# Optimization experiments

Measured on AMD Instinct MI355X. Metric: run time of the kernel, lower is better.

## Reference

```python
import jax, jax.numpy as jnp
import numpy as np

DIM_Q = 512
DIM_K = 512
DIM_V = 512
NUM_HEADS = 8
EPS = 1e-5


def _layer_norm(x, g, b):
    m = jnp.mean(x, axis=-1, keepdims=True)
    v = jnp.mean(jnp.square(x - m), axis=-1, keepdims=True)
    return (x - m) * jax.lax.rsqrt(v + EPS) * g + b


def setup_inputs() -> dict:
    key = jax.random.key(0)
    ks = jax.random.split(key, 12)
    B, Sq, Sk = 32, 512, 512
    s_q = 1.0 / np.sqrt(DIM_Q)
    s_v = 1.0 / np.sqrt(DIM_V)
    return {
        "Q": jax.random.normal(ks[0], (B, Sq, DIM_Q), jnp.float32),
        "K": jax.random.normal(ks[1], (B, Sk, DIM_K), jnp.float32),
        "Wq": jax.random.normal(ks[2], (DIM_Q, DIM_V), jnp.float32) * s_q,
        "bq": jnp.zeros((DIM_V,), jnp.float32),
        "Wk": jax.random.normal(ks[3], (DIM_K, DIM_V), jnp.float32) * s_q,
        "bk": jnp.zeros((DIM_V,), jnp.float32),
        "Wv": jax.random.normal(ks[4], (DIM_K, DIM_V), jnp.float32) * s_q,
        "bv": jnp.zeros((DIM_V,), jnp.float32),
        "Wo": jax.random.normal(ks[5], (DIM_V, DIM_V), jnp.float32) * s_v,
        "bo": jnp.zeros((DIM_V,), jnp.float32),
        "ln0_g": jnp.ones((DIM_V,), jnp.float32),
        "ln0_b": jnp.zeros((DIM_V,), jnp.float32),
        "ln1_g": jnp.ones((DIM_V,), jnp.float32),
        "ln1_b": jnp.zeros((DIM_V,), jnp.float32),
    }


def reference(Q, K, Wq, bq, Wk, bk, Wv, bv, Wo, bo, ln0_g, ln0_b, ln1_g, ln1_b):
    B, Sq, _ = Q.shape
    Sk = K.shape[1]
    H = NUM_HEADS
    dh = DIM_V // H
    q = Q @ Wq + bq  # [B, Sq, V]
    k = K @ Wk + bk  # [B, Sk, V]
    v = K @ Wv + bv  # [B, Sk, V]
    # split(dim_split, 2) + cat(dim 0) == standard head split
    qh = q.reshape(B, Sq, H, dh)
    kh = k.reshape(B, Sk, H, dh)
    vh = v.reshape(B, Sk, H, dh)
    # NOTE: original scales by sqrt(dim_V), not sqrt(head_dim)
    scores = jnp.einsum("bqhd,bkhd->bhqk", qh, kh) / np.sqrt(DIM_V)
    A = jax.nn.softmax(scores, axis=-1)  # [B, H, Sq, Sk]
    oh = qh + jnp.einsum("bhqk,bkhd->bqhd", A, vh)  # residual inside heads
    O = oh.reshape(B, Sq, DIM_V)  # cat heads back along feature dim
    O = _layer_norm(O, ln0_g, ln0_b)
    O = O + jax.nn.relu(O @ Wo + bo)
    O = _layer_norm(O, ln1_g, ln1_b)
    return O
```

## Files before the change

### kernel.cpp

```cpp
#include <hip/hip_runtime.h>

#define NB 32
#define SEQ 512
#define DIM 512
#define NH 8
#define DH 64
#define MTOT (NB*SEQ)

typedef __attribute__((ext_vector_type(8))) __bf16 bf16x8;
typedef __attribute__((ext_vector_type(8))) short s16x8;
typedef __attribute__((ext_vector_type(4))) float f32x4;
typedef __attribute__((ext_vector_type(16))) float f32x16;
typedef __attribute__((ext_vector_type(4))) unsigned u32x4;

__device__ __forceinline__ float bf2f(short u) {
    union { float f; unsigned u; } x; x.u = ((unsigned)(unsigned short)u) << 16; return x.f;
}
__device__ __forceinline__ short f2bf(float f) {
    union { float f; unsigned u; } x; x.f = f;
    unsigned r = x.u + 0x7FFFu + ((x.u >> 16) & 1u);
    return (short)(r >> 16);
}

#define MFMA16(a,b,c) __builtin_amdgcn_mfma_f32_16x16x32_bf16(a,b,c,0,0,0)
#define MFMA32(a,b,c) __builtin_amdgcn_mfma_f32_32x32x16_bf16(a,b,c,0,0,0)

__device__ __forceinline__ void gload_lds16(const void* g, void* l) {
    __builtin_amdgcn_global_load_lds(
        (const __attribute__((address_space(1))) unsigned int*)g,
        (__attribute__((address_space(3))) unsigned int*)l, 16, 0, 0);
}
__device__ __forceinline__ unsigned cvt_pk_bf16(float lo, float hi) {
    unsigned r;
    asm("v_cvt_pk_bf16_f32 %0, %1, %2" : "=v"(r) : "v"(lo), "v"(hi));
    return r;
}

__global__ __launch_bounds__(256) void k_wprep(
    const float* __restrict__ Wq, const float* __restrict__ Wk,
    const float* __restrict__ Wv, const float* __restrict__ Wo,
    short* __restrict__ Wt)
{
    __shared__ float t[64][65];
    const float* W = blockIdx.z==0?Wq: blockIdx.z==1?Wk: blockIdx.z==2?Wv:Wo;
    short* out = Wt + (size_t)blockIdx.z*DIM*DIM;
    int k0 = blockIdx.x*64, n0 = blockIdx.y*64;
    int c = threadIdx.x & 63, r4 = threadIdx.x >> 6;
    #pragma unroll
    for (int i=0;i<16;i++){ int r = i*4 + r4; t[r][c] = W[(size_t)(k0+r)*DIM + n0 + c]; }
    __syncthreads();
    #pragma unroll
    for (int i=0;i<16;i++){ int r = i*4 + r4; out[(size_t)(n0+r)*DIM + k0 + c] = f2bf(t[c][r]); }
}

__global__ __launch_bounds__(256) void k_projqkv(
    const float* __restrict__ Q, const float* __restrict__ K,
    const short* __restrict__ Wt,
    const float* __restrict__ bq, const float* __restrict__ bk, const float* __restrict__ bv,
    short* __restrict__ qb, short* __restrict__ kb, short* __restrict__ vT)
{
    __shared__ short lds[17408];
    short* As = lds;
    short* Bs = lds + 4096;
    const int tid = threadIdx.x;
    const int wave = tid >> 6, lane = tid & 63;
    const int z = blockIdx.z;
    const float* A   = (z==0) ? Q : K;
    const short* W   = Wt + z*(DIM*DIM);
    const float* bia = (z==0)?bq:(z==1)?bk:bv;
    const int m0 = blockIdx.x*128, n0 = blockIdx.y*128;

    const int arow = tid >> 1, acol = (tid & 1)*16;
    const float* Ag = A + (size_t)(m0+arow)*DIM + acol;
    const short* Bg = W + (size_t)(n0+arow)*DIM + acol;

    const int wr = (wave>>1)*64, wc = (wave&1)*64;
    const int fr = lane & 15, fk8 = (lane>>4)*8;

    f32x4 acc[4][4];
    #pragma unroll
    for (int i=0;i<4;i++)
        #pragma unroll
        for (int j=0;j<4;j++) acc[i][j] = (f32x4){0.f,0.f,0.f,0.f};

    float4 a0 = *(const float4*)(Ag);
    float4 a1 = *(const float4*)(Ag + 4);
    float4 a2 = *(const float4*)(Ag + 8);
    float4 a3 = *(const float4*)(Ag + 12);
    s16x8 w0  = *(const s16x8*)(Bg);
    s16x8 w1  = *(const s16x8*)(Bg + 8);

    for (int t=0; t<16; ++t) {
        u32x4 pA0 = { cvt_pk_bf16(a0.x,a0.y), cvt_pk_bf16(a0.z,a0.w),
                      cvt_pk_bf16(a1.x,a1.y), cvt_pk_bf16(a1.z,a1.w) };
        u32x4 pA1 = { cvt_pk_bf16(a2.x,a2.y), cvt_pk_bf16(a2.z,a2.w),
                      cvt_pk_bf16(a3.x,a3.y), cvt_pk_bf16(a3.z,a3.w) };
        __syncthreads();
        *(u32x4*)&As[arow*32 + acol]     = pA0;
        *(u32x4*)&As[arow*32 + acol + 8] = pA1;
        *(s16x8*)&Bs[arow*32 + acol]     = w0;
        *(s16x8*)&Bs[arow*32 + acol + 8] = w1;
        __syncthreads();
        if (t < 15) {
            const int k0 = (t+1)*32;
            a0 = *(const float4*)(Ag + k0);
            a1 = *(const float4*)(Ag + k0 + 4);
            a2 = *(const float4*)(Ag + k0 + 8);
            a3 = *(const float4*)(Ag + k0 + 12);
            w0 = *(const s16x8*)(Bg + k0);
            w1 = *(const s16x8*)(Bg + k0 + 8);
        }
        bf16x8 af[4], bfr[4];
        #pragma unroll
        for (int f=0;f<4;f++) af[f]  = *(const bf16x8*)&As[(wr + f*16 + fr)*32 + fk8];
        #pragma unroll
        for (int f=0;f<4;f++) bfr[f] = *(const bf16x8*)&Bs[(wc + f*16 + fr)*32 + fk8];
        #pragma unroll
        for (int i=0;i<4;i++)
            #pragma unroll
            for (int j=0;j<4;j++) acc[i][j] = MFMA16(af[i], bfr[j], acc[i][j]);
    }
    __syncthreads();

    const int r0 = (lane>>4)*4;
    #pragma unroll
    for (int i=0;i<4;i++)
        #pragma unroll
        for (int j=0;j<4;j++) {
            int row = wr + i*16 + r0;
            int col = wc + j*16 + fr;
            float bb = bia[n0 + col];
            #pragma unroll
            for (int r=0;r<4;r++) lds[(row+r)*136 + col] = f2bf(acc[i][j][r] + bb);
        }
    __syncthreads();
    if (z < 2) {
        short* out = (z==0)? qb : kb;
        int row = tid>>1, ch = (tid&1)*64;
        #pragma unroll
        for (int j=0;j<8;j++) {
            int col = ch + j*8;
            s16x8 v = *(s16x8*)&lds[row*136 + col];
            *(s16x8*)&out[(size_t)(m0+row)*DIM + n0 + col] = v;
        }
    } else {
        int c = tid>>1, sh = (tid&1)*64;
        int b = m0 >> 9;
        int h = (n0 + c) >> 6, d = (n0 + c) & 63;
        size_t base = ((size_t)(b*NH + h)*DH + d)*SEQ + (m0 & 511) + sh;
        #pragma unroll
        for (int i8=0;i8<8;i8++) {
            s16x8 tv;
            #pragma unroll
            for (int j=0;j<8;j++) tv[j] = lds[(sh + i8*8 + j)*136 + c];
            *(s16x8*)&vT[base + i8*8] = tv;
        }
    }
}

__global__ __launch_bounds__(256, 2) void k_attn(
    const short* __restrict__ qb, const short* __restrict__ kb,
    const short* __restrict__ vT, short* __restrict__ Oh)
{
    __shared__ short pool[9216];
    __shared__ float invLds[4][2][32];
    char* poolB = (char*)pool;
    const int tid = threadIdx.x, wave = tid>>6, lane = tid&63;
    const int l31 = lane & 31, hi = lane >> 5;
    const int b = blockIdx.z, h = blockIdx.y;
    const int bh = b*NH + h;
    const int bx = blockIdx.x;
    const float SCALE = 0.0441941738241592f;

    bf16x8 qf[2][4];
    #pragma unroll
    for (int u=0; u<2; ++u)
        #pragma unroll
        for (int d=0; d<4; ++d)
            qf[u][d] = *(const bf16x8*)&qb[(size_t)(b*SEQ + bx*256 + u*128 + wave*32 + l31)*DIM + h*DH + d*16 + hi*8];

    const short* gK0 = kb + (size_t)(b*SEQ + l31)*DIM + h*DH + wave*16 + hi*8;
    const short* gV0 = vT + ((size_t)bh*DH + (wave>>1)*32 + l31)*SEQ + (wave&1)*16 + hi*8;

    f32x16 o[2][2];
    #pragma unroll
    for (int u=0;u<2;u++)
        #pragma unroll
        for (int q=0;q<2;q++)
            #pragma unroll
            for (int r=0;r<16;r++) o[u][q][r]=0.f;
    float lsum[2] = {0.f, 0.f};

    gload_lds16(gK0,            poolB + wave*1024);
    gload_lds16(gV0,            poolB + 8192 + wave*1024);

    for (int kt=0; kt<16; ++kt) {
        const int p = kt & 1;
        __syncthreads();
        if (kt < 15) {
            gload_lds16(gK0 + (size_t)(kt+1)*32*DIM, poolB + (p^1)*4096 + wave*1024);
            gload_lds16(gV0 + (kt+1)*32,             poolB + 8192 + (p^1)*4096 + wave*1024);
        }
        const char* Kb = poolB + p*4096 + lane*16;
        bf16x8 kf0 = *(const bf16x8*)(Kb);
        bf16x8 kf1 = *(const bf16x8*)(Kb + 1024);
        bf16x8 kf2 = *(const bf16x8*)(Kb + 2048);
        bf16x8 kf3 = *(const bf16x8*)(Kb + 3072);
        const char* Vb = poolB + 8192 + p*4096 + lane*16;
        bf16x8 v00 = *(const bf16x8*)(Vb);
        bf16x8 v01 = *(const bf16x8*)(Vb + 1024);
        bf16x8 v10 = *(const bf16x8*)(Vb + 2048);
        bf16x8 v11 = *(const bf16x8*)(Vb + 3072);
        #pragma unroll
        for (int u=0; u<2; ++u) {
            f32x16 s;
            #pragma unroll
            for (int r=0;r<16;r++) s[r]=0.f;
            s = MFMA32(kf0, qf[u][0], s);
            s = MFMA32(kf1, qf[u][1], s);
            s = MFMA32(kf2, qf[u][2], s);
            s = MFMA32(kf3, qf[u][3], s);
            float pe[16];
            #pragma unroll
            for (int r=0;r<16;r++) { pe[r] = __expf(s[r]*SCALE - 3.0f); lsum[u] += pe[r]; }
            unsigned pk0 = cvt_pk_bf16(pe[0],  pe[1]);
            unsigned pk1 = cvt_pk_bf16(pe[2],  pe[3]);
            unsigned pk2 = cvt_pk_bf16(pe[4],  pe[5]);
            unsigned pk3 = cvt_pk_bf16(pe[6],  pe[7]);
            unsigned pk4 = cvt_pk_bf16(pe[8],  pe[9]);
            unsigned pk5 = cvt_pk_bf16(pe[10], pe[11]);
            unsigned pk6 = cvt_pk_bf16(pe[12], pe[13]);
            unsigned pk7 = cvt_pk_bf16(pe[14], pe[15]);
            asm("v_permlane32_swap_b32 %0, %1" : "+v"(pk0), "+v"(pk2));
            asm("v_permlane32_swap_b32 %0, %1" : "+v"(pk1), "+v"(pk3));
            asm("v_permlane32_swap_b32 %0, %1" : "+v"(pk4), "+v"(pk6));
            asm("v_permlane32_swap_b32 %0, %1" : "+v"(pk5), "+v"(pk7));
            u32x4 f0w = {pk0, pk1, pk2, pk3};
            u32x4 f1w = {pk4, pk5, pk6, pk7};
            bf16x8 F0 = __builtin_bit_cast(bf16x8, f0w);
            bf16x8 F1 = __builtin_bit_cast(bf16x8, f1w);
            o[u][0] = MFMA32(F0, v00, o[u][0]);
            o[u][0] = MFMA32(F1, v01, o[u][0]);
            o[u][1] = MFMA32(F0, v10, o[u][1]);
            o[u][1] = MFMA32(F1, v11, o[u][1]);
        }
    }
    float linv[2];
    #pragma unroll
    for (int u=0;u<2;u++) { float v = lsum[u]; v += __shfl_xor(v, 32); linv[u] = 1.0f / v; }
    __syncthreads();
    if (lane < 32) { invLds[wave][0][l31] = linv[0]; invLds[wave][1][l31] = linv[1]; }
    short* O = pool + wave*2304;
    #pragma unroll
    for (int u=0; u<2; ++u) {
        #pragma unroll
        for (int r=0;r<16;r++) {
            int q = (r&3) + 8*(r>>2) + 4*hi;
            float iq = invLds[wave][u][q];
            O[q*72 + l31]      = f2bf(o[u][0][r] * iq);
            O[q*72 + 32 + l31] = f2bf(o[u][1][r] * iq);
        }
        int rr = lane>>1, c0 = (lane&1)*32;
        size_t baseO = ((size_t)bh*SEQ + bx*256 + u*128 + wave*32 + rr)*DH + c0;
        #pragma unroll
        for (int j=0;j<4;j++) {
            s16x8 v = *(s16x8*)&O[rr*72 + c0 + j*8];
            *(s16x8*)&Oh[baseO + j*8] = v;
        }
    }
}

__global__ __launch_bounds__(256) void k_ln0(
    const short* __restrict__ qb, const short* __restrict__ Oh,
    const float* __restrict__ g, const float* __restrict__ bt,
    short* __restrict__ x0)
{
    int wave = threadIdx.x>>6, lane = threadIdx.x&63;
    int row = blockIdx.x*4 + wave;
    int b = row >> 9, s = row & 511;
    int f0 = lane*8;
    s16x8 qv = *(const s16x8*)&qb[(size_t)row*DIM + f0];
    int h = f0 >> 6, d = f0 & 63;
    s16x8 ov = *(const s16x8*)&Oh[((size_t)(b*NH+h)*SEQ + s)*DH + d];
    float x[8];
    float sm=0.f, sq=0.f;
    #pragma unroll
    for (int j=0;j<8;j++) { x[j] = bf2f(qv[j]) + bf2f(ov[j]); sm += x[j]; sq += x[j]*x[j]; }
    #pragma unroll
    for (int off=1; off<64; off<<=1) { sm += __shfl_xor(sm,off); sq += __shfl_xor(sq,off); }
    float mean = sm*(1.0f/512.0f);
    float var  = sq*(1.0f/512.0f) - mean*mean;
    float inv  = rsqrtf(var + 1e-5f);
    float4 g0 = *(const float4*)&g[f0],  g1 = *(const float4*)&g[f0+4];
    float4 t0 = *(const float4*)&bt[f0], t1 = *(const float4*)&bt[f0+4];
    s16x8 outv;
    outv[0]=f2bf((x[0]-mean)*inv*g0.x + t0.x); outv[1]=f2bf((x[1]-mean)*inv*g0.y + t0.y);
    outv[2]=f2bf((x[2]-mean)*inv*g0.z + t0.z); outv[3]=f2bf((x[3]-mean)*inv*g0.w + t0.w);
    outv[4]=f2bf((x[4]-mean)*inv*g1.x + t1.x); outv[5]=f2bf((x[5]-mean)*inv*g1.y + t1.y);
    outv[6]=f2bf((x[6]-mean)*inv*g1.z + t1.z); outv[7]=f2bf((x[7]-mean)*inv*g1.w + t1.w);
    *(s16x8*)&x0[(size_t)row*DIM + f0] = outv;
}

__global__ __launch_bounds__(512) void k_gemmy_ln(
    const short* __restrict__ x0, const short* __restrict__ Wto,
    const float* __restrict__ bo,
    const float* __restrict__ g, const float* __restrict__ bt,
    float* __restrict__ out)
{
    __shared__ __align__(16) char pool[73728];
    const int tid = threadIdx.x;
    const int wave = tid >> 6, lane = tid & 63;
    const int fr = lane & 15, g4 = lane >> 4;

    int L = ((int)blockIdx.x & 7)*32 + ((int)blockIdx.x >> 3);
    const int m0 = L*64;

    size_t srcA = 0;
    if (wave < 4) {
        int r = tid>>2, c = tid&3;
        srcA = (size_t)(m0 + r)*DIM + ((c ^ ((r>>1)&3))<<3);
    }
    size_t srcB[4];
    #pragma unroll
    for (int i=0;i<4;i++) {
        int s = i*512 + tid, r = s>>2, c = s&3;
        srcB[i] = (size_t)r*DIM + ((c ^ ((r>>1)&3))<<3);
    }

    f32x4 acc[16];
    #pragma unroll
    for (int j=0;j<16;j++) acc[j] = (f32x4){0.f,0.f,0.f,0.f};

#define GSTAGE(T, BUF) do { \
        const short* As_ = x0  + (T)*32; \
        const short* Bs_ = Wto + (T)*32; \
        if (wave < 4) gload_lds16(As_ + srcA, pool + (BUF)*4096 + wave*1024); \
        char* dB_ = pool + 8192 + (BUF)*32768; \
        gload_lds16(Bs_ + srcB[0], dB_ +     0 + wave*1024); \
        gload_lds16(Bs_ + srcB[1], dB_ +  8192 + wave*1024); \
        gload_lds16(Bs_ + srcB[2], dB_ + 16384 + wave*1024); \
        gload_lds16(Bs_ + srcB[3], dB_ + 24576 + wave*1024); \
    } while(0)

    GSTAGE(0, 0);
    __syncthreads();

    int cur = 0;
    for (int t=0; t<16; ++t) {
        if (t < 15) GSTAGE(t+1, cur^1);
        const char* pA = pool + cur*4096;
        const char* pB = pool + 8192 + cur*32768;
        int R = (wave>>1)*16 + fr;
        bf16x8 af = *(const bf16x8*)(pA + R*64 + ((g4 ^ ((R>>1)&3))<<4));
        #pragma unroll
        for (int j=0;j<16;j++) {
            int Rb = (wave&1)*256 + j*16 + fr;
            bf16x8 bf = *(const bf16x8*)(pB + Rb*64 + ((g4 ^ ((Rb>>1)&3))<<4));
            acc[j] = MFMA16(af, bf, acc[j]);
        }
        __syncthreads();
        cur ^= 1;
    }
#undef GSTAGE

    short (*Lo)[520] = (short(*)[520])pool;
    {
        int wrow = (wave>>1)*16 + g4*4;
        int cbase = (wave&1)*256;
        #pragma unroll
        for (int j=0;j<16;j++) {
            int col = cbase + j*16 + fr;
            float bb = bo[col];
            #pragma unroll
            for (int r=0;r<4;r++) {
                float vv = acc[j][r] + bb;
                vv = vv > 0.f ? vv : 0.f;
                Lo[wrow + r][col] = f2bf(vv);
            }
        }
    }
    __syncthreads();

    int f0 = lane*8;
    float4 gg0 = *(const float4*)&g[f0],  gg1 = *(const float4*)&g[f0+4];
    float4 tt0 = *(const float4*)&bt[f0], tt1 = *(const float4*)&bt[f0+4];
    #pragma unroll
    for (int rr=0; rr<8; ++rr) {
        int row = wave*8 + rr;
        s16x8 rv = *(s16x8*)&Lo[row][f0];
        s16x8 xv = *(const s16x8*)&x0[(size_t)(m0+row)*DIM + f0];
        float x[8];
        float sm=0.f, sq=0.f;
        #pragma unroll
        for (int j=0;j<8;j++) { x[j] = bf2f(rv[j]) + bf2f(xv[j]); sm += x[j]; sq += x[j]*x[j]; }
        #pragma unroll
        for (int off=1; off<64; off<<=1) { sm += __shfl_xor(sm,off); sq += __shfl_xor(sq,off); }
        float mean = sm*(1.0f/512.0f);
        float var  = sq*(1.0f/512.0f) - mean*mean;
        float inv  = rsqrtf(var + 1e-5f);
        float4 o0, o1;
        o0.x=(x[0]-mean)*inv*gg0.x + tt0.x; o0.y=(x[1]-mean)*inv*gg0.y + tt0.y;
        o0.z=(x[2]-mean)*inv*gg0.z + tt0.z; o0.w=(x[3]-mean)*inv*gg0.w + tt0.w;
        o1.x=(x[4]-mean)*inv*gg1.x + tt1.x; o1.y=(x[5]-mean)*inv*gg1.y + tt1.y;
        o1.z=(x[6]-mean)*inv*gg1.z + tt1.z; o1.w=(x[7]-mean)*inv*gg1.w + tt1.w;
        *(float4*)&out[(size_t)(m0+row)*DIM + f0]     = o0;
        *(float4*)&out[(size_t)(m0+row)*DIM + f0 + 4] = o1;
    }
}

extern "C" void kernel_launch(void* const* d_in, const int* in_sizes, int n_in,
                              void* d_out, int out_size, void* d_ws, size_t ws_size,
                              hipStream_t stream)
{
    const float* Q  = (const float*)d_in[0];
    const float* K  = (const float*)d_in[1];
    const float* Wq = (const float*)d_in[2];
    const float* bq = (const float*)d_in[3];
    const float* Wk = (const float*)d_in[4];
    const float* bk = (const float*)d_in[5];
    const float* Wv = (const float*)d_in[6];
    const float* bv = (const float*)d_in[7];
    const float* Wo = (const float*)d_in[8];
    const float* bo = (const float*)d_in[9];
    const float* g0 = (const float*)d_in[10];
    const float* be0= (const float*)d_in[11];
    const float* g1 = (const float*)d_in[12];
    const float* be1= (const float*)d_in[13];
    float* out = (float*)d_out;

    char* ws = (char*)d_ws;
    size_t off = 0;
    short* Wt = (short*)(ws + off); off += (size_t)4*DIM*DIM*2;
    short* qb = (short*)(ws + off); off += (size_t)MTOT*DIM*2;
    short* kb = (short*)(ws + off); off += (size_t)MTOT*DIM*2;
    short* vT = (short*)(ws + off); off += (size_t)MTOT*DIM*2;
    short* Oh = (short*)(ws + off); off += (size_t)MTOT*DIM*2;
    short* x0 = vT;

    k_wprep   <<<dim3(8,8,4),   256, 0, stream>>>(Wq,Wk,Wv,Wo,Wt);
    k_projqkv <<<dim3(128,4,3), 256, 0, stream>>>(Q,K,Wt,bq,bk,bv,qb,kb,vT);
    k_attn    <<<dim3(2,NH,NB), 256, 0, stream>>>(qb,kb,vT,Oh);
    k_ln0     <<<dim3(MTOT/4),  256, 0, stream>>>(qb,Oh,g0,be0,x0);
    k_gemmy_ln<<<dim3(256),     512, 0, stream>>>(x0, Wt + (size_t)3*DIM*DIM, bo, g1, be1, out);
}
```

Measured before the change: 132.7 us.

## Load projection tiles directly to LDS with swizzle and convert A in registers

The QKV projection GEMM now stages A (fp32) and W (bf16) tiles through direct global-to-LDS loads, with an XOR swizzle on the fp32 A tile, instead of loading into registers and storing to LDS. The fp32-to-bf16 conversion of A moves to after the LDS read, just before the MFMAs. The aim is to cut register staging and VGPR pressure and to overlap the next stage's loads with compute. The cost is twice the LDS footprint and LDS read bandwidth for A, since it is kept in fp32, and the prefetch is single-buffered between barriers.

```diff
diff --git a/kernel.cpp b/kernel.cpp
--- a/kernel.cpp
+++ b/kernel.cpp
@@ -59,9 +59,10 @@
     const float* __restrict__ bq, const float* __restrict__ bk, const float* __restrict__ bv,
     short* __restrict__ qb, short* __restrict__ kb, short* __restrict__ vT)
 {
-    __shared__ short lds[17408];
-    short* As = lds;
-    short* Bs = lds + 4096;
+    __shared__ __align__(16) char pool[34816];
+    short* lds = (short*)pool;
+    char* As = pool;
+    char* Bs = pool + 16384;
     const int tid = threadIdx.x;
     const int wave = tid >> 6, lane = tid & 63;
     const int z = blockIdx.z;
@@ -70,12 +71,31 @@
     const float* bia = (z==0)?bq:(z==1)?bk:bv;
     const int m0 = blockIdx.x*128, n0 = blockIdx.y*128;
 
-    const int arow = tid >> 1, acol = (tid & 1)*16;
-    const float* Ag = A + (size_t)(m0+arow)*DIM + acol;
-    const short* Bg = W + (size_t)(n0+arow)*DIM + acol;
+    const float* srcA[4];
+    #pragma unroll
+    for (int i=0;i<4;i++) {
+        int P = i*256 + tid, r = P>>3, pc = P&7, lc = pc ^ (r&7);
+        srcA[i] = A + (size_t)(m0+r)*DIM + lc*4;
+    }
+    const short* srcB[2];
+    #pragma unroll
+    for (int i=0;i<2;i++) {
+        int P = i*256 + tid, r = P>>2, c = P&3;
+        srcB[i] = W + (size_t)(n0+r)*DIM + c*8;
+    }
+
+#define PSTAGE(T) do { \
+        const int k0_ = (T)*32; \
+        gload_lds16(srcA[0] + k0_, As +         wave*1024); \
+        gload_lds16(srcA[1] + k0_, As +  4096 + wave*1024); \
+        gload_lds16(srcA[2] + k0_, As +  8192 + wave*1024); \
+        gload_lds16(srcA[3] + k0_, As + 12288 + wave*1024); \
+        gload_lds16(srcB[0] + k0_, Bs +         wave*1024); \
+        gload_lds16(srcB[1] + k0_, Bs +  4096 + wave*1024); \
+    } while(0)
 
     const int wr = (wave>>1)*64, wc = (wave&1)*64;
-    const int fr = lane & 15, fk8 = (lane>>4)*8;
+    const int fr = lane & 15, kg = lane >> 4;
 
     f32x4 acc[4][4];
     #pragma unroll
@@ -83,43 +103,37 @@
         #pragma unroll
         for (int j=0;j<4;j++) acc[i][j] = (f32x4){0.f,0.f,0.f,0.f};
 
-    float4 a0 = *(const float4*)(Ag);
-    float4 a1 = *(const float4*)(Ag + 4);
-    float4 a2 = *(const float4*)(Ag + 8);
-    float4 a3 = *(const float4*)(Ag + 12);
-    s16x8 w0  = *(const s16x8*)(Bg);
-    s16x8 w1  = *(const s16x8*)(Bg + 8);
+    PSTAGE(0);
 
     for (int t=0; t<16; ++t) {
-        u32x4 pA0 = { cvt_pk_bf16(a0.x,a0.y), cvt_pk_bf16(a0.z,a0.w),
-                      cvt_pk_bf16(a1.x,a1.y), cvt_pk_bf16(a1.z,a1.w) };
-        u32x4 pA1 = { cvt_pk_bf16(a2.x,a2.y), cvt_pk_bf16(a2.z,a2.w),
-                      cvt_pk_bf16(a3.x,a3.y), cvt_pk_bf16(a3.z,a3.w) };
         __syncthreads();
-        *(u32x4*)&As[arow*32 + acol]     = pA0;
-        *(u32x4*)&As[arow*32 + acol + 8] = pA1;
-        *(s16x8*)&Bs[arow*32 + acol]     = w0;
-        *(s16x8*)&Bs[arow*32 + acol + 8] = w1;
+        float4 alo[4], ahi[4];
+        #pragma unroll
+        for (int f=0; f<4; ++f) {
+            int R = wr + f*16 + fr;
+            const char* base = As + R*128;
+            alo[f] = *(const float4*)(base + ((((kg<<1)  ) ^ (R&7))<<4));
+            ahi[f] = *(const float4*)(base + ((((kg<<1)|1) ^ (R&7))<<4));
+        }
+        bf16x8 bfr[4];
+        #pragma unroll
+        for (int f=0; f<4; ++f)
+            bfr[f] = *(const bf16x8*)(Bs + (wc + f*16 + fr)*64 + kg*16);
         __syncthreads();
-        if (t < 15) {
-            const int k0 = (t+1)*32;
-            a0 = *(const float4*)(Ag + k0);
-            a1 = *(const float4*)(Ag + k0 + 4);
-            a2 = *(const float4*)(Ag + k0 + 8);
-            a3 = *(const float4*)(Ag + k0 + 12);
-            w0 = *(const s16x8*)(Bg + k0);
-            w1 = *(const s16x8*)(Bg + k0 + 8);
-        }
-        bf16x8 af[4], bfr[4];
-        #pragma unroll
-        for (int f=0;f<4;f++) af[f]  = *(const bf16x8*)&As[(wr + f*16 + fr)*32 + fk8];
-        #pragma unroll
-        for (int f=0;f<4;f++) bfr[f] = *(const bf16x8*)&Bs[(wc + f*16 + fr)*32 + fk8];
+        if (t < 15) PSTAGE(t+1);
+        bf16x8 af[4];
+        #pragma unroll
+        for (int f=0; f<4; ++f) {
+            u32x4 pk = { cvt_pk_bf16(alo[f].x, alo[f].y), cvt_pk_bf16(alo[f].z, alo[f].w),
+                         cvt_pk_bf16(ahi[f].x, ahi[f].y), cvt_pk_bf16(ahi[f].z, ahi[f].w) };
+            af[f] = __builtin_bit_cast(bf16x8, pk);
+        }
         #pragma unroll
         for (int i=0;i<4;i++)
             #pragma unroll
             for (int j=0;j<4;j++) acc[i][j] = MFMA16(af[i], bfr[j], acc[i][j]);
     }
+#undef PSTAGE
     __syncthreads();
 
     const int r0 = (lane>>4)*4;
```

Result: slower. 139.7 us (+5.2%).
